# Optimization experiments

Measured on AMD Instinct MI355X. Metric: run time of the kernel, lower is better.

## Reference

```python
import jax, jax.numpy as jnp
import numpy as np

LN_EPS = 1e-5


def _layer_norm(h, g, b):
    mu = jnp.mean(h, axis=-1, keepdims=True)
    var = jnp.var(h, axis=-1, keepdims=True)
    return (h - mu) * jax.lax.rsqrt(var + LN_EPS) * g + b


def _gin_layer(x, src, dst, n, w1, b1, w2, b2, ln_g, ln_b):
    # scatter-add aggregation: agg[i] = sum_{(s,d): d==i} x[s]
    agg = jax.ops.segment_sum(x[src], dst, num_segments=n)
    h = x + agg  # eps = 0 (GINConv default)
    h = jnp.maximum(h @ w1 + b1, 0.0) @ w2 + b2
    h = _layer_norm(h, ln_g, ln_b)
    return jnp.maximum(h, 0.0)  # ReLU; dropout is identity at eval


def setup_inputs() -> dict:
    key = jax.random.key(0)
    ks = jax.random.split(key, 24)
    N, E, G = 100000, 1600000, 128
    F_IN, H, P = 128, 256, 128

    def lin(k, fi, fo):
        s = 1.0 / np.sqrt(fi)
        kw, kb = jax.random.split(k)
        return (jax.random.uniform(kw, (fi, fo), jnp.float32, -s, s),
                jax.random.uniform(kb, (fo,), jnp.float32, -s, s))

    x = jax.random.normal(ks[0], (N, F_IN), jnp.float32)
    edge_index = jax.random.randint(ks[1], (2, E), 0, N, jnp.int32)
    batch = jnp.sort(jax.random.randint(ks[2], (N,), 0, G, jnp.int32))

    w1_0, b1_0 = lin(ks[3], F_IN, H)
    w2_0, b2_0 = lin(ks[4], H, H)
    w1_1, b1_1 = lin(ks[5], H, H)
    w2_1, b2_1 = lin(ks[6], H, H)
    gate_w1, gate_b1 = lin(ks[7], H, P)
    gate_w2, gate_b2 = lin(ks[8], P, 1)
    cls_w1, cls_b1 = lin(ks[9], H, P)
    cls_w2, cls_b2 = lin(ks[10], P, 2)

    return dict(
        x=x, edge_index=edge_index, batch=batch, num_graphs=G,
        w1_0=w1_0, b1_0=b1_0, w2_0=w2_0, b2_0=b2_0,
        ln_g0=jnp.ones((H,), jnp.float32), ln_b0=jnp.zeros((H,), jnp.float32),
        w1_1=w1_1, b1_1=b1_1, w2_1=w2_1, b2_1=b2_1,
        ln_g1=jnp.ones((H,), jnp.float32), ln_b1=jnp.zeros((H,), jnp.float32),
        gate_w1=gate_w1, gate_b1=gate_b1, gate_w2=gate_w2, gate_b2=gate_b2,
        cls_w1=cls_w1, cls_b1=cls_b1, cls_w2=cls_w2, cls_b2=cls_b2,
    )


def reference(x, edge_index, batch, num_graphs,
              w1_0, b1_0, w2_0, b2_0, ln_g0, ln_b0,
              w1_1, b1_1, w2_1, b2_1, ln_g1, ln_b1,
              gate_w1, gate_b1, gate_w2, gate_b2,
              cls_w1, cls_b1, cls_w2, cls_b2):
    n = x.shape[0]
    src, dst = edge_index[0], edge_index[1]

    h = _gin_layer(x, src, dst, n, w1_0, b1_0, w2_0, b2_0, ln_g0, ln_b0)
    h = _gin_layer(h, src, dst, n, w1_1, b1_1, w2_1, b2_1, ln_g1, ln_b1)

    # GlobalAttention pooling: per-graph scatter-softmax over gate scores
    gate = jnp.maximum(h @ gate_w1 + gate_b1, 0.0) @ gate_w2 + gate_b2  # [N,1]
    gate = gate[:, 0]
    gmax = jax.ops.segment_max(gate, batch, num_segments=num_graphs)
    e = jnp.exp(gate - gmax[batch])
    den = jax.ops.segment_sum(e, batch, num_segments=num_graphs)
    alpha = e / den[batch]  # [N]
    pooled = jax.ops.segment_sum(h * alpha[:, None], batch, num_segments=num_graphs)

    # classifier (dropout = identity at eval)
    out = jnp.maximum(pooled @ cls_w1 + cls_b1, 0.0) @ cls_w2 + cls_b2
    return out  # [num_graphs, 2]
```

## Files before the change

kernel.cpp:

```cpp
#include <hip/hip_runtime.h>
#include <math.h>

#define H 256

typedef float f32x4 __attribute__((ext_vector_type(4)));
typedef _Float16 half8 __attribute__((ext_vector_type(8)));
typedef _Float16 half4 __attribute__((ext_vector_type(4)));
typedef _Float16 half2v __attribute__((ext_vector_type(2)));
typedef unsigned long long u64;

__device__ inline unsigned pkh(float a, float b) {
    auto t = __builtin_amdgcn_cvt_pkrtz(a, b);
    union { decltype(t) h; unsigned u; } v; v.h = t; return v.u;
}
__device__ inline ushort f2h(float f) {
    union { _Float16 h; ushort u; } v; v.h = (_Float16)f; return v.u;
}
__device__ inline void gload_lds16(const void* gp, void* lp) {
    __builtin_amdgcn_global_load_lds(
        (const __attribute__((address_space(1))) unsigned int*)gp,
        (__attribute__((address_space(3))) unsigned int*)lp,
        16, 0, 0);
}


__global__ void count_deg(const int* __restrict__ dst, int* __restrict__ deg, int E) {
    int e = blockIdx.x * blockDim.x + threadIdx.x;
    if (e < E) atomicAdd(&deg[dst[e]], 1);
}

__global__ void scan_block(const int* __restrict__ deg, int* __restrict__ row,
                           int* __restrict__ btot, int n) {
    __shared__ int wsum[16];
    int tid = threadIdx.x;
    int lane = tid & 63, wid = tid >> 6;
    int i = blockIdx.x * 1024 + tid;
    int v = (i < n) ? deg[i] : 0;
    int x = v;
    #pragma unroll
    for (int off = 1; off < 64; off <<= 1) {
        int t = __shfl_up(x, off, 64);
        if (lane >= off) x += t;
    }
    if (lane == 63) wsum[wid] = x;
    __syncthreads();
    int wexc = 0;
    for (int w = 0; w < wid; ++w) wexc += wsum[w];
    int incl = wexc + x;
    if (i < n) row[i + 1] = incl;
    if (tid == 1023) btot[blockIdx.x] = incl;
}

__global__ void scan_tops(const int* __restrict__ btot, int* __restrict__ boff, int nb) {
    __shared__ int wsum[16];
    int tid = threadIdx.x;
    int lane = tid & 63, wid = tid >> 6;
    int v = (tid < nb) ? btot[tid] : 0;
    int x = v;
    #pragma unroll
    for (int off = 1; off < 64; off <<= 1) {
        int t = __shfl_up(x, off, 64);
        if (lane >= off) x += t;
    }
    if (lane == 63) wsum[wid] = x;
    __syncthreads();
    int wexc = 0;
    for (int w = 0; w < wid; ++w) wexc += wsum[w];
    if (tid < nb) boff[tid] = wexc + x - v;
}

__global__ void scan_add(const int* __restrict__ boff, int* __restrict__ row, int n) {
    int i = blockIdx.x * 1024 + threadIdx.x;
    if (i == 0) row[0] = 0;
    if (i < n) row[i + 1] += boff[blockIdx.x];
}

__global__ void fill_csr(const int* __restrict__ src, const int* __restrict__ dst,
                         const int* __restrict__ row, int* __restrict__ cursor,
                         int* __restrict__ srcl, int E) {
    int e = blockIdx.x * blockDim.x + threadIdx.x;
    if (e < E) {
        int d = dst[e];
        int p = atomicAdd(&cursor[d], 1);
        srcl[row[d] + p] = src[e];
    }
}


__global__ void prep_weights(const float* __restrict__ w10, const float* __restrict__ w20,
                             const float* __restrict__ w11, const float* __restrict__ w21,
                             const float* __restrict__ gw1,
                             ushort* __restrict__ w1t0, ushort* __restrict__ w2t0,
                             ushort* __restrict__ w1t1, ushort* __restrict__ w2t1,
                             ushort* __restrict__ gw1t) {
    int i = blockIdx.x * 256 + threadIdx.x;
    if (i < 32768) {
        int k = i >> 8, n = i & 255;
        w1t0[n * 128 + k] = f2h(w10[i]);
    } else if (i < 32768 + 65536) {
        int j = i - 32768; int k = j >> 8, n = j & 255;
        w2t0[n * 256 + k] = f2h(w20[j]);
    } else if (i < 32768 + 131072) {
        int j = i - (32768 + 65536); int k = j >> 8, n = j & 255;
        w1t1[n * 256 + k] = f2h(w11[j]);
    } else if (i < 32768 + 196608) {
        int j = i - (32768 + 131072); int k = j >> 8, n = j & 255;
        w2t1[n * 256 + k] = f2h(w21[j]);
    } else if (i < 32768 + 196608 + 32768) {
        int j = i - (32768 + 196608); int k = j >> 7, n = j & 127;
        gw1t[n * 256 + k] = f2h(gw1[j]);
    }
}


__global__ void xcast(const float* __restrict__ x, u64* __restrict__ xb, int n4) {
    int i = blockIdx.x * 256 + threadIdx.x;
    if (i < n4) {
        f32x4 v = ((const f32x4*)x)[i];
        xb[i] = (u64)pkh(v[0], v[1]) | ((u64)pkh(v[2], v[3]) << 32);
    }
}


__global__ void aggregate0(const unsigned* __restrict__ xb, const int* __restrict__ row,
                           const int* __restrict__ srcl, unsigned* __restrict__ out, int N) {
    int n = blockIdx.x * 4 + (threadIdx.x >> 6);
    int f = threadIdx.x & 63;
    if (n >= N) return;
    union U { unsigned u; half2v h; };
    int s0 = row[n], s1 = row[n + 1];
    U a[16];
    a[0].u = xb[(size_t)n * 64 + f];
    #pragma unroll
    for (int q = 1; q < 16; ++q) a[q].h = (half2v)0;
    for (int base = s0; base < s1; base += 64) {
        int cnt = s1 - base; if (cnt > 64) cnt = 64;
        int idx = srcl[base + (f < cnt ? f : 0)];
        int j = 0;
        for (; j + 15 < cnt; j += 16) {
            U u[16];
            #pragma unroll
            for (int q = 0; q < 16; ++q)
                u[q].u = xb[(size_t)__builtin_amdgcn_readlane(idx, j + q) * 64 + f];
            #pragma unroll
            for (int q = 0; q < 16; ++q) a[q].h += u[q].h;
        }
        for (; j + 3 < cnt; j += 4) {
            U u[4];
            #pragma unroll
            for (int q = 0; q < 4; ++q)
                u[q].u = xb[(size_t)__builtin_amdgcn_readlane(idx, j + q) * 64 + f];
            #pragma unroll
            for (int q = 0; q < 4; ++q) a[q].h += u[q].h;
        }
        for (; j < cnt; ++j) {
            U u0; u0.u = xb[(size_t)__builtin_amdgcn_readlane(idx, j) * 64 + f];
            a[0].h += u0.h;
        }
    }
    #pragma unroll
    for (int q = 0; q < 8; ++q) a[q].h += a[q + 8].h;
    #pragma unroll
    for (int q = 0; q < 4; ++q) a[q].h += a[q + 4].h;
    a[0].h += a[2].h; a[1].h += a[3].h;
    a[0].h += a[1].h;
    int of = (((f >> 2) ^ (n & 7)) << 2) | (f & 3);
    out[(size_t)n * 64 + of] = a[0].u;
}

__global__ void aggregate1(const u64* __restrict__ h, const int* __restrict__ row,
                           const int* __restrict__ srcl, u64* __restrict__ out, int N) {
    int n = blockIdx.x * 4 + (threadIdx.x >> 6);
    int f = threadIdx.x & 63;
    if (n >= N) return;
    union U { u64 u; half4 h; };
    int s0 = row[n], s1 = row[n + 1];
    U a[16];
    a[0].u = h[(size_t)n * 64 + f];
    #pragma unroll
    for (int q = 1; q < 16; ++q) a[q].h = (half4)0;
    for (int base = s0; base < s1; base += 64) {
        int cnt = s1 - base; if (cnt > 64) cnt = 64;
        int idx = srcl[base + (f < cnt ? f : 0)];
        int j = 0;
        for (; j + 15 < cnt; j += 16) {
            U u[16];
            #pragma unroll
            for (int q = 0; q < 16; ++q)
                u[q].u = h[(size_t)__builtin_amdgcn_readlane(idx, j + q) * 64 + f];
            #pragma unroll
            for (int q = 0; q < 16; ++q) a[q].h += u[q].h;
        }
        for (; j + 3 < cnt; j += 4) {
            U u[4];
            #pragma unroll
            for (int q = 0; q < 4; ++q)
                u[q].u = h[(size_t)__builtin_amdgcn_readlane(idx, j + q) * 64 + f];
            #pragma unroll
            for (int q = 0; q < 4; ++q) a[q].h += u[q].h;
        }
        for (; j < cnt; ++j) {
            U u0; u0.u = h[(size_t)__builtin_amdgcn_readlane(idx, j) * 64 + f];
            a[0].h += u0.h;
        }
    }
    #pragma unroll
    for (int q = 0; q < 8; ++q) a[q].h += a[q + 8].h;
    #pragma unroll
    for (int q = 0; q < 4; ++q) a[q].h += a[q + 4].h;
    a[0].h += a[2].h; a[1].h += a[3].h;
    a[0].h += a[1].h;
    int of = (((f >> 1) ^ (n & 7)) << 1) | (f & 1);
    out[(size_t)n * 64 + of] = a[0].u;
}


template<int K1, bool DO_GATE>
__global__ void __launch_bounds__(256, 3) mlp_mfma(
        const ushort* __restrict__ hsum, const ushort* __restrict__ w1t,
        const float* __restrict__ b1, const ushort* __restrict__ w2t,
        const float* __restrict__ b2, const float* __restrict__ lng,
        const float* __restrict__ lnb, ushort* __restrict__ hout,
        const ushort* __restrict__ gw1t, const float* __restrict__ gb1,
        const float* __restrict__ gw2, const float* __restrict__ gb2,
        float* __restrict__ gate, int N) {
    constexpr int ROWB = K1 * 2;
    constexpr int TILEB = 64 * ROWB;
    __shared__ ushort hsum_t[64 * K1];
    __shared__ ushort hid[64 * 256];
    __shared__ float2 lnred[4 * 64];
    __shared__ float gred[4 * 64];
    int tid = threadIdx.x;
    int w = tid >> 6, lane = tid & 63;
    int ll = lane & 15, kg = lane >> 4;
    int n0 = blockIdx.x * 64;

    {
        const char* gs = (const char*)hsum;
        #pragma unroll
        for (int r = 0; r < TILEB / 4096; ++r) {
            int off = r * 4096 + w * 1024;
            int myoff = off + lane * 16;
            int mynode = myoff / ROWB;
            int inrow = myoff - mynode * ROWB;
            int gn = n0 + mynode; if (gn >= N) gn = N - 1;
            gload_lds16(gs + (size_t)gn * ROWB + inrow, (char*)hsum_t + off);
        }
    }
    __syncthreads();

    constexpr int KC1 = K1 / 32;
    f32x4 acc[4][4];
    #pragma unroll
    for (int f = 0; f < 4; ++f)
        #pragma unroll
        for (int nt = 0; nt < 4; ++nt) acc[f][nt] = (f32x4){0.f, 0.f, 0.f, 0.f};
    {
        half8 wcur[4];
        #pragma unroll
        for (int f = 0; f < 4; ++f)
            wcur[f] = *(const half8*)(w1t + (size_t)(16 * (4 * w + f) + ll) * K1 + kg * 8);
        #pragma unroll
        for (int kc = 0; kc < KC1; ++kc) {
            half8 wnx[4];
            if (kc + 1 < KC1) {
                #pragma unroll
                for (int f = 0; f < 4; ++f)
                    wnx[f] = *(const half8*)(w1t + (size_t)(16 * (4 * w + f) + ll) * K1 + (kc + 1) * 32 + kg * 8);
            }
            half8 bfr[4];
            #pragma unroll
            for (int nt = 0; nt < 4; ++nt) {
                int node = 16 * nt + ll;
                bfr[nt] = *(const half8*)((char*)hsum_t + node * ROWB +
                                          (((kc * 4 + kg) ^ (node & 7)) << 4));
            }
            #pragma unroll
            for (int f = 0; f < 4; ++f)
                #pragma unroll
                for (int nt = 0; nt < 4; ++nt)
                    acc[f][nt] = __builtin_amdgcn_mfma_f32_16x16x32_f16(wcur[f], bfr[nt], acc[f][nt], 0, 0, 0);
            if (kc + 1 < KC1) {
                #pragma unroll
                for (int f = 0; f < 4; ++f) wcur[f] = wnx[f];
            }
        }
    }
    #pragma unroll
    for (int f = 0; f < 4; ++f) {
        int feat0 = 16 * (4 * w + f) + 4 * kg;
        f32x4 bq = *(const f32x4*)(b1 + feat0);
        int fb = feat0 * 2;
        #pragma unroll
        for (int nt = 0; nt < 4; ++nt) {
            int node = 16 * nt + ll;
            float v0 = fmaxf(acc[f][nt][0] + bq[0], 0.f);
            float v1 = fmaxf(acc[f][nt][1] + bq[1], 0.f);
            float v2 = fmaxf(acc[f][nt][2] + bq[2], 0.f);
            float v3 = fmaxf(acc[f][nt][3] + bq[3], 0.f);
            unsigned lo = pkh(v0, v1), hi2 = pkh(v2, v3);
            int sb = node * 512 + ((((fb >> 4) ^ (node & 7))) << 4) + (fb & 15);
            *(u64*)((char*)hid + sb) = (u64)lo | ((u64)hi2 << 32);
        }
    }
    __syncthreads();

    #pragma unroll
    for (int f = 0; f < 4; ++f)
        #pragma unroll
        for (int nt = 0; nt < 4; ++nt) acc[f][nt] = (f32x4){0.f, 0.f, 0.f, 0.f};
    {
        half8 wcur[4];
        #pragma unroll
        for (int f = 0; f < 4; ++f)
            wcur[f] = *(const half8*)(w2t + (size_t)(16 * (4 * w + f) + ll) * 256 + kg * 8);
        #pragma unroll
        for (int kc = 0; kc < 8; ++kc) {
            half8 wnx[4];
            if (kc < 7) {
                #pragma unroll
                for (int f = 0; f < 4; ++f)
                    wnx[f] = *(const half8*)(w2t + (size_t)(16 * (4 * w + f) + ll) * 256 + (kc + 1) * 32 + kg * 8);
            }
            half8 bfr[4];
            int fb = kc * 64 + kg * 16;
            #pragma unroll
            for (int nt = 0; nt < 4; ++nt) {
                int node = 16 * nt + ll;
                int sb = node * 512 + ((((fb >> 4) ^ (node & 7))) << 4);
                bfr[nt] = *(const half8*)((char*)hid + sb);
            }
            #pragma unroll
            for (int f = 0; f < 4; ++f)
                #pragma unroll
                for (int nt = 0; nt < 4; ++nt)
                    acc[f][nt] = __builtin_amdgcn_mfma_f32_16x16x32_f16(wcur[f], bfr[nt], acc[f][nt], 0, 0, 0);
            if (kc < 7) {
                #pragma unroll
                for (int f = 0; f < 4; ++f) wcur[f] = wnx[f];
            }
        }
    }

    float sA[4] = {0, 0, 0, 0}, sB[4] = {0, 0, 0, 0};
    #pragma unroll
    for (int f = 0; f < 4; ++f) {
        int feat0 = 16 * (4 * w + f) + 4 * kg;
        f32x4 bq = *(const f32x4*)(b2 + feat0);
        #pragma unroll
        for (int nt = 0; nt < 4; ++nt) {
            #pragma unroll
            for (int r = 0; r < 4; ++r) {
                float v = acc[f][nt][r] + bq[r];
                acc[f][nt][r] = v;
                sA[nt] += v; sB[nt] += v * v;
            }
        }
    }
    #pragma unroll
    for (int nt = 0; nt < 4; ++nt) {
        sA[nt] += __shfl_xor(sA[nt], 16, 64); sA[nt] += __shfl_xor(sA[nt], 32, 64);
        sB[nt] += __shfl_xor(sB[nt], 16, 64); sB[nt] += __shfl_xor(sB[nt], 32, 64);
    }
    if (lane < 16) {
        #pragma unroll
        for (int nt = 0; nt < 4; ++nt)
            lnred[w * 64 + nt * 16 + ll] = make_float2(sA[nt], sB[nt]);
    }
    __syncthreads();

    float mu[4], rs[4];
    #pragma unroll
    for (int nt = 0; nt < 4; ++nt) {
        float a = 0.f, b = 0.f;
        #pragma unroll
        for (int wv = 0; wv < 4; ++wv) {
            float2 t = lnred[wv * 64 + nt * 16 + ll];
            a += t.x; b += t.y;
        }
        float m = a * (1.f / 256.f);
        mu[nt] = m;
        rs[nt] = rsqrtf(b * (1.f / 256.f) - m * m + 1e-5f);
    }

    #pragma unroll
    for (int f = 0; f < 4; ++f) {
        int feat0 = 16 * (4 * w + f) + 4 * kg;
        f32x4 gq = *(const f32x4*)(lng + feat0);
        f32x4 bq = *(const f32x4*)(lnb + feat0);
        int fb = feat0 * 2;
        #pragma unroll
        for (int nt = 0; nt < 4; ++nt) {
            int node = 16 * nt + ll;
            int n = n0 + node;
            float v0 = fmaxf((acc[f][nt][0] - mu[nt]) * rs[nt] * gq[0] + bq[0], 0.f);
            float v1 = fmaxf((acc[f][nt][1] - mu[nt]) * rs[nt] * gq[1] + bq[1], 0.f);
            float v2 = fmaxf((acc[f][nt][2] - mu[nt]) * rs[nt] * gq[2] + bq[2], 0.f);
            float v3 = fmaxf((acc[f][nt][3] - mu[nt]) * rs[nt] * gq[3] + bq[3], 0.f);
            unsigned lo = pkh(v0, v1), hi2 = pkh(v2, v3);
            u64 pv = (u64)lo | ((u64)hi2 << 32);
            if (n < N)
                *(u64*)(hout + (size_t)n * 256 + feat0) = pv;
            if (DO_GATE) {
                int sb = node * 512 + ((((fb >> 4) ^ (node & 7))) << 4) + (fb & 15);
                *(u64*)((char*)hid + sb) = pv;
            }
        }
    }

    if (DO_GATE) {
        __syncthreads();
        f32x4 ga[2][4];
        #pragma unroll
        for (int f = 0; f < 2; ++f)
            #pragma unroll
            for (int nt = 0; nt < 4; ++nt) ga[f][nt] = (f32x4){0.f, 0.f, 0.f, 0.f};
        half8 wcur[2];
        #pragma unroll
        for (int f = 0; f < 2; ++f)
            wcur[f] = *(const half8*)(gw1t + (size_t)(16 * (2 * w + f) + ll) * 256 + kg * 8);
        #pragma unroll
        for (int kc = 0; kc < 8; ++kc) {
            half8 wnx[2];
            if (kc < 7) {
                #pragma unroll
                for (int f = 0; f < 2; ++f)
                    wnx[f] = *(const half8*)(gw1t + (size_t)(16 * (2 * w + f) + ll) * 256 + (kc + 1) * 32 + kg * 8);
            }
            half8 bfr[4];
            int fb = kc * 64 + kg * 16;
            #pragma unroll
            for (int nt = 0; nt < 4; ++nt) {
                int node = 16 * nt + ll;
                int sb = node * 512 + ((((fb >> 4) ^ (node & 7))) << 4);
                bfr[nt] = *(const half8*)((char*)hid + sb);
            }
            #pragma unroll
            for (int f = 0; f < 2; ++f)
                #pragma unroll
                for (int nt = 0; nt < 4; ++nt)
                    ga[f][nt] = __builtin_amdgcn_mfma_f32_16x16x32_f16(wcur[f], bfr[nt], ga[f][nt], 0, 0, 0);
            if (kc < 7) {
                #pragma unroll
                for (int f = 0; f < 2; ++f) wcur[f] = wnx[f];
            }
        }
        float gp[4] = {0, 0, 0, 0};
        #pragma unroll
        for (int f = 0; f < 2; ++f) {
            int feat0 = 16 * (2 * w + f) + 4 * kg;
            f32x4 gbq = *(const f32x4*)(gb1 + feat0);
            f32x4 gwq = *(const f32x4*)(gw2 + feat0);
            #pragma unroll
            for (int nt = 0; nt < 4; ++nt)
                #pragma unroll
                for (int r = 0; r < 4; ++r)
                    gp[nt] += fmaxf(ga[f][nt][r] + gbq[r], 0.f) * gwq[r];
        }
        #pragma unroll
        for (int nt = 0; nt < 4; ++nt) {
            gp[nt] += __shfl_xor(gp[nt], 16, 64);
            gp[nt] += __shfl_xor(gp[nt], 32, 64);
        }
        if (lane < 16) {
            #pragma unroll
            for (int nt = 0; nt < 4; ++nt)
                gred[w * 64 + nt * 16 + ll] = gp[nt];
        }
        __syncthreads();
        if (w == 0 && lane < 16) {
            #pragma unroll
            for (int nt = 0; nt < 4; ++nt) {
                int n = n0 + 16 * nt + ll;
                if (n < N) {
                    float gs = gred[nt * 16 + ll] + gred[64 + nt * 16 + ll] +
                               gred[128 + nt * 16 + ll] + gred[192 + nt * 16 + ll];
                    gate[n] = gs + gb2[0];
                }
            }
        }
    }
}


__global__ void boundaries(const int* __restrict__ batch, int* __restrict__ gstart,
                           int* __restrict__ gend, int N) {
    int i = blockIdx.x * blockDim.x + threadIdx.x;
    if (i >= N) return;
    int b = batch[i];
    if (i == 0 || batch[i - 1] != b) gstart[b] = i;
    if (i == N - 1 || batch[i + 1] != b) gend[b] = i + 1;
}


__global__ void gate_stats(const float* __restrict__ gate, const int* __restrict__ gstart,
                           const int* __restrict__ gend, float* __restrict__ ebuf,
                           float* __restrict__ den) {
    __shared__ float red[256];
    int g = blockIdx.x;
    int tid = threadIdx.x;
    int s = gstart[g], e = gend[g];
    float lmax = -INFINITY;
    for (int n = s + tid; n < e; n += 256) lmax = fmaxf(lmax, gate[n]);
    red[tid] = lmax;
    __syncthreads();
    for (int off = 128; off > 0; off >>= 1) {
        if (tid < off) red[tid] = fmaxf(red[tid], red[tid + off]);
        __syncthreads();
    }
    float gmax = red[0];
    __syncthreads();
    float lsum = 0.f;
    for (int n = s + tid; n < e; n += 256) {
        float ev = expf(gate[n] - gmax);
        ebuf[n] = ev;
        lsum += ev;
    }
    red[tid] = lsum;
    __syncthreads();
    for (int off = 128; off > 0; off >>= 1) {
        if (tid < off) red[tid] += red[tid + off];
        __syncthreads();
    }
    if (tid == 0) den[g] = red[0];
}

__global__ void pool_feat(const ushort* __restrict__ h, const float* __restrict__ ebuf,
                          const float* __restrict__ den, const int* __restrict__ gstart,
                          const int* __restrict__ gend, float* __restrict__ pooled) {
    __shared__ float2 pl[512];
    int g = blockIdx.x, c = blockIdx.y;
    int tid = threadIdx.x;
    int fq = tid & 31, ng = tid >> 5;
    int s = gstart[g], e = gend[g];
    float2 acc = make_float2(0.f, 0.f);
    for (int n = s + ng; n < e; n += 16) {
        float wv = ebuf[n];
        union { unsigned u; half2v h2; } v;
        v.u = *(const unsigned*)(h + (size_t)n * 256 + c * 64 + fq * 2);
        acc.x += (float)v.h2[0] * wv;
        acc.y += (float)v.h2[1] * wv;
    }
    pl[tid] = acc;
    __syncthreads();
    if (tid < 32) {
        float2 a = pl[tid];
        #pragma unroll
        for (int q = 1; q < 16; ++q) {
            float2 t = pl[q * 32 + tid];
            a.x += t.x; a.y += t.y;
        }
        float d = (e > s) ? den[g] : 1.f;
        float inv = 1.f / d;
        pooled[g * 256 + c * 64 + fq * 2]     = (e > s) ? a.x * inv : 0.f;
        pooled[g * 256 + c * 64 + fq * 2 + 1] = (e > s) ? a.y * inv : 0.f;
    }
}

__global__ void cls_kernel(const float* __restrict__ pooled,
                           const float* __restrict__ cw1, const float* __restrict__ cb1,
                           const float* __restrict__ cw2, const float* __restrict__ cb2,
                           float* __restrict__ out) {
    __shared__ float pl[256];
    __shared__ float c2[256];
    int g = blockIdx.x;
    int tid = threadIdx.x;
    pl[tid] = pooled[g * 256 + tid];
    pl[tid + 128] = pooled[g * 256 + 128 + tid];
    __syncthreads();
    float a = cb1[tid];
    #pragma unroll 2
    for (int k = 0; k < H; ++k) a = fmaf(pl[k], cw1[(size_t)k * 128 + tid], a);
    a = fmaxf(a, 0.f);
    c2[tid * 2 + 0] = a * cw2[tid * 2 + 0];
    c2[tid * 2 + 1] = a * cw2[tid * 2 + 1];
    __syncthreads();
    if (tid < 2) {
        float sres = cb2[tid];
        for (int p = 0; p < 128; ++p) sres += c2[p * 2 + tid];
        out[g * 2 + tid] = sres;
    }
}


extern "C" void kernel_launch(void* const* d_in, const int* in_sizes, int n_in,
                              void* d_out, int out_size, void* d_ws, size_t ws_size,
                              hipStream_t stream) {
    const float* x     = (const float*)d_in[0];
    const int*   ei    = (const int*)d_in[1];
    const int*   batch = (const int*)d_in[2];
    const float* w1_0  = (const float*)d_in[4];
    const float* b1_0  = (const float*)d_in[5];
    const float* w2_0  = (const float*)d_in[6];
    const float* b2_0  = (const float*)d_in[7];
    const float* lng0  = (const float*)d_in[8];
    const float* lnb0  = (const float*)d_in[9];
    const float* w1_1  = (const float*)d_in[10];
    const float* b1_1  = (const float*)d_in[11];
    const float* w2_1  = (const float*)d_in[12];
    const float* b2_1  = (const float*)d_in[13];
    const float* lng1  = (const float*)d_in[14];
    const float* lnb1  = (const float*)d_in[15];
    const float* gw1   = (const float*)d_in[16];
    const float* gb1   = (const float*)d_in[17];
    const float* gw2   = (const float*)d_in[18];
    const float* gb2   = (const float*)d_in[19];
    const float* cw1   = (const float*)d_in[20];
    const float* cb1   = (const float*)d_in[21];
    const float* cw2   = (const float*)d_in[22];
    const float* cb2   = (const float*)d_in[23];

    int N = in_sizes[2];
    int E = in_sizes[1] / 2;
    int G = out_size / 2;
    const int* src = ei;
    const int* dst = ei + E;

    char* p = (char*)d_ws;
    auto alloc = [&](size_t bytes) {
        char* r = p;
        p += (bytes + 255) & ~(size_t)255;
        return r;
    };
    int*    row    = (int*)alloc((size_t)(N + 1) * 4);
    int*    cursor = (int*)alloc((size_t)N * 4);
    int*    srcl   = (int*)alloc((size_t)E * 4);
    float*  gate   = (float*)alloc((size_t)N * 4);
    float*  ebuf   = (float*)alloc((size_t)N * 4);
    float*  den    = (float*)alloc((size_t)G * 4);
    float*  pooled = (float*)alloc((size_t)G * 256 * 4);
    int*    gstart = (int*)alloc((size_t)G * 4);
    int*    gend   = (int*)alloc((size_t)G * 4);
    int*    btot   = (int*)alloc(1024 * 4);
    int*    boff   = (int*)alloc(1024 * 4);
    ushort* xb     = (ushort*)alloc((size_t)N * 128 * 2);
    ushort* hsum0  = (ushort*)alloc((size_t)N * 128 * 2);
    ushort* h1     = (ushort*)alloc((size_t)N * 256 * 2);
    ushort* hsum1  = (ushort*)alloc((size_t)N * 256 * 2);
    ushort* h2     = (ushort*)alloc((size_t)N * 256 * 2);
    ushort* w1t0   = (ushort*)alloc(128 * 256 * 2);
    ushort* w2t0   = (ushort*)alloc(256 * 256 * 2);
    ushort* w1t1   = (ushort*)alloc(256 * 256 * 2);
    ushort* w2t1   = (ushort*)alloc(256 * 256 * 2);
    ushort* gw1t   = (ushort*)alloc(128 * 256 * 2);

    prep_weights<<<1024, 256, 0, stream>>>(w1_0, w2_0, w1_1, w2_1, gw1,
                                           w1t0, w2t0, w1t1, w2t1, gw1t);
    xcast<<<(N * 32 + 255) / 256, 256, 0, stream>>>(x, (u64*)xb, N * 32);
    hipMemsetAsync(cursor, 0, (size_t)N * 4, stream);
    count_deg<<<(E + 255) / 256, 256, 0, stream>>>(dst, cursor, E);
    int nb = (N + 1023) / 1024;
    scan_block<<<nb, 1024, 0, stream>>>(cursor, row, btot, N);
    scan_tops<<<1, 1024, 0, stream>>>(btot, boff, nb);
    scan_add<<<nb, 1024, 0, stream>>>(boff, row, N);
    hipMemsetAsync(cursor, 0, (size_t)N * 4, stream);
    fill_csr<<<(E + 255) / 256, 256, 0, stream>>>(src, dst, row, cursor, srcl, E);

    int agg_blocks = (N + 3) / 4;
    int mlp_blocks = (N + 63) / 64;
    aggregate0<<<agg_blocks, 256, 0, stream>>>((const unsigned*)xb, row, srcl,
                                               (unsigned*)hsum0, N);
    mlp_mfma<128, false><<<mlp_blocks, 256, 0, stream>>>(
        hsum0, w1t0, b1_0, w2t0, b2_0, lng0, lnb0, h1,
        nullptr, nullptr, nullptr, nullptr, nullptr, N);
    aggregate1<<<agg_blocks, 256, 0, stream>>>((const u64*)h1, row, srcl,
                                               (u64*)hsum1, N);
    mlp_mfma<256, true><<<mlp_blocks, 256, 0, stream>>>(
        hsum1, w1t1, b1_1, w2t1, b2_1, lng1, lnb1, h2,
        gw1t, gb1, gw2, gb2, gate, N);
    hipMemsetAsync(gstart, 0, (size_t)G * 4, stream);
    hipMemsetAsync(gend, 0, (size_t)G * 4, stream);
    boundaries<<<(N + 255) / 256, 256, 0, stream>>>(batch, gstart, gend, N);
    gate_stats<<<G, 256, 0, stream>>>(gate, gstart, gend, ebuf, den);
    pool_feat<<<dim3(G, 4), 512, 0, stream>>>(h2, ebuf, den, gstart, gend, pooled);
    cls_kernel<<<G, 128, 0, stream>>>(pooled, cw1, cb1, cw2, cb2, (float*)d_out);
}
```

Measured before the change: 575.9 us.

## Build CSR via two-level bucket sort instead of global atomics

Replaces the global-atomic degree count, three-kernel scan and random-scatter CSR fill with a coarse bucket histogram, a binning pass that writes (dst,src) pairs into per-bucket regions using LDS atomics, and a per-bucket kernel that computes local degrees, row offsets and srcl placement in shared memory. The aim is to cut contended global atomics and scattered writes during CSR construction. In exchange it adds an 8-byte-per-edge pairs buffer and an extra pass over the edges. With N=100000 the bucket count is 196, so only 196 blocks run fill_bucket, each serially handling about 8K edges.

```diff
diff --git a/kernel.cpp b/kernel.cpp
--- a/kernel.cpp
+++ b/kernel.cpp
@@ -24,65 +24,113 @@
 }
 
 
-__global__ void count_deg(const int* __restrict__ dst, int* __restrict__ deg, int E) {
-    int e = blockIdx.x * blockDim.x + threadIdx.x;
-    if (e < E) atomicAdd(&deg[dst[e]], 1);
-}
-
-__global__ void scan_block(const int* __restrict__ deg, int* __restrict__ row,
-                           int* __restrict__ btot, int n) {
-    __shared__ int wsum[16];
+__global__ void bucket_hist(const int* __restrict__ dst, int* __restrict__ bktCnt,
+                            int E, int shift) {
+    __shared__ int h[256];
     int tid = threadIdx.x;
-    int lane = tid & 63, wid = tid >> 6;
-    int i = blockIdx.x * 1024 + tid;
-    int v = (i < n) ? deg[i] : 0;
+    h[tid] = 0;
+    __syncthreads();
+    for (int e = blockIdx.x * 256 + tid; e < E; e += gridDim.x * 256)
+        atomicAdd(&h[dst[e] >> shift], 1);
+    __syncthreads();
+    if (h[tid]) atomicAdd(&bktCnt[tid], h[tid]);
+}
+
+__global__ void scan_buckets(const int* __restrict__ cnt, int* __restrict__ base,
+                             int* __restrict__ cur, int nb) {
+    __shared__ int ws[4];
+    int tid = threadIdx.x, lane = tid & 63, wid = tid >> 6;
+    int v = (tid < nb) ? cnt[tid] : 0;
     int x = v;
     #pragma unroll
     for (int off = 1; off < 64; off <<= 1) {
         int t = __shfl_up(x, off, 64);
         if (lane >= off) x += t;
     }
-    if (lane == 63) wsum[wid] = x;
+    if (lane == 63) ws[wid] = x;
     __syncthreads();
     int wexc = 0;
-    for (int w = 0; w < wid; ++w) wexc += wsum[w];
-    int incl = wexc + x;
-    if (i < n) row[i + 1] = incl;
-    if (tid == 1023) btot[blockIdx.x] = incl;
-}
-
-__global__ void scan_tops(const int* __restrict__ btot, int* __restrict__ boff, int nb) {
-    __shared__ int wsum[16];
+    for (int w = 0; w < wid; ++w) wexc += ws[w];
+    int excl = wexc + x - v;
+    if (tid < nb) { base[tid] = excl; cur[tid] = excl; }
+    if (tid == nb - 1) base[nb] = excl + v;
+}
+
+#define BIN_EPT 16
+__global__ void __launch_bounds__(256) bin_pass(
+        const int* __restrict__ src, const int* __restrict__ dst,
+        int* __restrict__ bktCur, u64* __restrict__ pairs, int E, int shift) {
+    __shared__ int hist[256];
+    __shared__ int base_s[256];
     int tid = threadIdx.x;
-    int lane = tid & 63, wid = tid >> 6;
-    int v = (tid < nb) ? btot[tid] : 0;
-    int x = v;
+    hist[tid] = 0;
+    __syncthreads();
+    int e0 = blockIdx.x * (256 * BIN_EPT);
+    int mys[BIN_EPT], myd[BIN_EPT], myslot[BIN_EPT];
+    #pragma unroll
+    for (int i = 0; i < BIN_EPT; ++i) {
+        int e = e0 + i * 256 + tid;
+        if (e < E) {
+            mys[i] = src[e];
+            myd[i] = dst[e];
+            myslot[i] = atomicAdd(&hist[myd[i] >> shift], 1);
+        }
+    }
+    __syncthreads();
+    base_s[tid] = hist[tid] ? atomicAdd(&bktCur[tid], hist[tid]) : 0;
+    __syncthreads();
+    #pragma unroll
+    for (int i = 0; i < BIN_EPT; ++i) {
+        int e = e0 + i * 256 + tid;
+        if (e < E)
+            pairs[base_s[myd[i] >> shift] + myslot[i]] =
+                ((u64)(unsigned)myd[i] << 32) | (unsigned)mys[i];
+    }
+}
+
+__global__ void __launch_bounds__(256) fill_bucket(
+        const u64* __restrict__ pairs, const int* __restrict__ bktBase,
+        int* __restrict__ row, int* __restrict__ srcl, int N, int shift, int NB) {
+    __shared__ int deg[512];
+    __shared__ int ws[4];
+    int b = blockIdx.x;
+    int n0 = b << shift;
+    int nodes = (1 << shift); if (n0 + nodes > N) nodes = N - n0;
+    int e0 = bktBase[b], e1 = bktBase[b + 1];
+    int tid = threadIdx.x, lane = tid & 63, wid = tid >> 6;
+    deg[tid] = 0; deg[tid + 256] = 0;
+    __syncthreads();
+    for (int e = e0 + tid; e < e1; e += 256) {
+        int d = (int)(pairs[e] >> 32) - n0;
+        atomicAdd(&deg[d], 1);
+    }
+    __syncthreads();
+    int a0 = deg[2 * tid], a1 = deg[2 * tid + 1];
+    int ps = a0 + a1;
+    int x = ps;
     #pragma unroll
     for (int off = 1; off < 64; off <<= 1) {
         int t = __shfl_up(x, off, 64);
         if (lane >= off) x += t;
     }
-    if (lane == 63) wsum[wid] = x;
+    if (lane == 63) ws[wid] = x;
     __syncthreads();
     int wexc = 0;
-    for (int w = 0; w < wid; ++w) wexc += wsum[w];
-    if (tid < nb) boff[tid] = wexc + x - v;
-}
-
-__global__ void scan_add(const int* __restrict__ boff, int* __restrict__ row, int n) {
-    int i = blockIdx.x * 1024 + threadIdx.x;
-    if (i == 0) row[0] = 0;
-    if (i < n) row[i + 1] += boff[blockIdx.x];
-}
-
-__global__ void fill_csr(const int* __restrict__ src, const int* __restrict__ dst,
-                         const int* __restrict__ row, int* __restrict__ cursor,
-                         int* __restrict__ srcl, int E) {
-    int e = blockIdx.x * blockDim.x + threadIdx.x;
-    if (e < E) {
-        int d = dst[e];
-        int p = atomicAdd(&cursor[d], 1);
-        srcl[row[d] + p] = src[e];
+    for (int w = 0; w < wid; ++w) wexc += ws[w];
+    int p0 = wexc + x - ps;
+    int p1 = p0 + a0;
+    if (2 * tid < nodes)     row[n0 + 2 * tid]     = e0 + p0;
+    if (2 * tid + 1 < nodes) row[n0 + 2 * tid + 1] = e0 + p1;
+    if (b == NB - 1 && tid == 0) row[N] = e1;
+    __syncthreads();
+    deg[2 * tid] = e0 + p0;
+    deg[2 * tid + 1] = e0 + p1;
+    __syncthreads();
+    for (int e = e0 + tid; e < e1; e += 256) {
+        u64 pr = pairs[e];
+        int d = (int)(pr >> 32) - n0;
+        int p = atomicAdd(&deg[d], 1);
+        srcl[p] = (int)(pr & 0xffffffffu);
     }
 }
 
@@ -616,6 +664,10 @@
     const int* src = ei;
     const int* dst = ei + E;
 
+    int shift = 9;
+    while ((((N - 1) >> shift) + 1) > 256) shift++;
+    int NB = ((N - 1) >> shift) + 1;
+
     char* p = (char*)d_ws;
     auto alloc = [&](size_t bytes) {
         char* r = p;
@@ -623,16 +675,17 @@
         return r;
     };
     int*    row    = (int*)alloc((size_t)(N + 1) * 4);
-    int*    cursor = (int*)alloc((size_t)N * 4);
     int*    srcl   = (int*)alloc((size_t)E * 4);
+    u64*    pairs  = (u64*)alloc((size_t)E * 8);
+    int*    bktCnt = (int*)alloc(256 * 4);
+    int*    bktBase= (int*)alloc(257 * 4);
+    int*    bktCur = (int*)alloc(256 * 4);
     float*  gate   = (float*)alloc((size_t)N * 4);
     float*  ebuf   = (float*)alloc((size_t)N * 4);
     float*  den    = (float*)alloc((size_t)G * 4);
     float*  pooled = (float*)alloc((size_t)G * 256 * 4);
     int*    gstart = (int*)alloc((size_t)G * 4);
     int*    gend   = (int*)alloc((size_t)G * 4);
-    int*    btot   = (int*)alloc(1024 * 4);
-    int*    boff   = (int*)alloc(1024 * 4);
     ushort* xb     = (ushort*)alloc((size_t)N * 128 * 2);
     ushort* hsum0  = (ushort*)alloc((size_t)N * 128 * 2);
     ushort* h1     = (ushort*)alloc((size_t)N * 256 * 2);
@@ -647,14 +700,11 @@
     prep_weights<<<1024, 256, 0, stream>>>(w1_0, w2_0, w1_1, w2_1, gw1,
                                            w1t0, w2t0, w1t1, w2t1, gw1t);
     xcast<<<(N * 32 + 255) / 256, 256, 0, stream>>>(x, (u64*)xb, N * 32);
-    hipMemsetAsync(cursor, 0, (size_t)N * 4, stream);
-    count_deg<<<(E + 255) / 256, 256, 0, stream>>>(dst, cursor, E);
-    int nb = (N + 1023) / 1024;
-    scan_block<<<nb, 1024, 0, stream>>>(cursor, row, btot, N);
-    scan_tops<<<1, 1024, 0, stream>>>(btot, boff, nb);
-    scan_add<<<nb, 1024, 0, stream>>>(boff, row, N);
-    hipMemsetAsync(cursor, 0, (size_t)N * 4, stream);
-    fill_csr<<<(E + 255) / 256, 256, 0, stream>>>(src, dst, row, cursor, srcl, E);
+    hipMemsetAsync(bktCnt, 0, 256 * 4, stream);
+    bucket_hist<<<1024, 256, 0, stream>>>(dst, bktCnt, E, shift);
+    scan_buckets<<<1, 256, 0, stream>>>(bktCnt, bktBase, bktCur, NB);
+    bin_pass<<<(E + 4095) / 4096, 256, 0, stream>>>(src, dst, bktCur, pairs, E, shift);
+    fill_bucket<<<NB, 256, 0, stream>>>(pairs, bktBase, row, srcl, N, shift, NB);
 
     int agg_blocks = (N + 3) / 4;
     int mlp_blocks = (N + 63) / 64;
```

Result: faster. 503.0 us (-12.7%).
